# Kernel optimization log

Hardware: AMD Instinct MI355X
Metric: run time of the kernel (lower is better)

## Reference

```python
import jax, jax.numpy as jnp
import numpy as np

GAMMA = 0.05
EPS = 1e-12
H, NH, HD = 768, 12, 64

def _lin(x, W, b):
    return x @ W.T + b

def _pproc(x, W, b):
    # LRP gamma-rule projection: forward value equals _lin(x, W, b); gradient flows through the gamma-modified layer times a detached ratio.
    z = _lin(x, W, b)
    zp = _lin(x, W + GAMMA * jnp.clip(W, 0.0, None), b + GAMMA * jnp.clip(b, 0.0, None))
    return zp * jax.lax.stop_gradient(z / zp)

def setup_inputs() -> dict:
    key = jax.random.key(0)
    ks = jax.random.split(key, 9)
    s = 0.02
    d = {"hidden_states": jax.random.normal(ks[0], (2, 2048, H), jnp.float32)}
    for i, n in enumerate(["q", "k", "v", "o"]):
        d["W" + n] = jax.random.normal(ks[1 + 2 * i], (H, H), jnp.float32) * s
        d["b" + n] = jax.random.normal(ks[2 + 2 * i], (H,), jnp.float32) * s
    return d

def reference(hidden_states, Wq, bq, Wk, bk, Wv, bv, Wo, bo):
    B, S, _ = hidden_states.shape
    def heads(x):  # [B,S,H] -> [B,NH,S,HD]
        return x.reshape(B, S, NH, HD).transpose(0, 2, 1, 3)
    q = heads(_pproc(hidden_states, Wq, bq))
    k = heads(_pproc(hidden_states, Wk, bk))
    v = heads(_pproc(hidden_states, Wv, bv))
    # NOTE: source has NO 1/sqrt(d_head) scaling on the scores
    scores = jnp.einsum("bhsd,bhtd->bhst", q, k)
    probs = jax.lax.stop_gradient(jax.nn.softmax(scores, axis=-1))  # detach_kq branch
    ctx = jnp.einsum("bhst,bhtd->bhsd", probs, v).transpose(0, 2, 1, 3).reshape(B, S, H)
    # BertSelfOutput.pforward: gamma-modified dense applied directly (no pproc ratio)
    pWo = Wo + GAMMA * jnp.clip(Wo, 0.0, None)
    pbo = bo + GAMMA * jnp.clip(bo, 0.0, None)
    y = _lin(ctx, pWo, pbo) + hidden_states
    # 'nowb' LayerNorm with detached mean and std (torch.std -> unbiased, ddof=1)
    mean = jax.lax.stop_gradient(jnp.mean(y, axis=-1, keepdims=True))
    std = jax.lax.stop_gradient(jnp.std(y, axis=-1, keepdims=True, ddof=1))
    out = (y - mean) / (std + EPS)
    return out, probs
```

## Files before the change

kernel.cpp:

```cpp
#include <hip/hip_runtime.h>

#define GAMMA 0.05f
#define LNEPS 1e-12f
#define HDIMT 768
#define SDIM  2048
#define NHEAD 12
#define HDHEAD 64
#define MTOT  4096
#define BHEADS 24
#define OUT0E ((size_t)MTOT * HDIMT)
#define NXEL  ((size_t)MTOT * HDIMT)
#define WNEL  ((size_t)HDIMT * HDIMT)
#define NEATT ((size_t)BHEADS * SDIM * HDHEAD)

typedef __attribute__((ext_vector_type(8))) short short8;
typedef __attribute__((ext_vector_type(4))) float f32x4;
typedef __attribute__((ext_vector_type(16))) float f32x16;

#define MFMA16(a, b, c) __builtin_amdgcn_mfma_f32_16x16x32_bf16((a), (b), (c), 0, 0, 0)
#define MFMA32(a, b, c) __builtin_amdgcn_mfma_f32_32x32x16_bf16((a), (b), (c), 0, 0, 0)

__device__ __forceinline__ float bf2f(unsigned short u) {
    union { unsigned int i; float f; } c; c.i = ((unsigned int)u) << 16; return c.f;
}
__device__ __forceinline__ unsigned short f2bf(float f) {
    union { float f; unsigned int i; } c; c.f = f;
    unsigned int i = c.i;
    i += 0x7FFFu + ((i >> 16) & 1u);
    return (unsigned short)(i >> 16);
}
__device__ __forceinline__ void splitbf(float v, unsigned short& h, unsigned short& l) {
    h = f2bf(v);
    l = f2bf(v - bf2f(h));
}

__device__ __forceinline__ void load8f(const void* p, size_t idx, int isbf, float* r) {
    if (isbf) {
        const unsigned short* b = (const unsigned short*)p + idx;
        uint4 u = *(const uint4*)b;
        const unsigned short* pu = (const unsigned short*)&u;
        #pragma unroll
        for (int j = 0; j < 8; ++j) r[j] = bf2f(pu[j]);
    } else {
        const float* f = (const float*)p + idx;
        float4 a = *(const float4*)f, c = *(const float4*)(f + 4);
        r[0] = a.x; r[1] = a.y; r[2] = a.z; r[3] = a.w;
        r[4] = c.x; r[5] = c.y; r[6] = c.z; r[7] = c.w;
    }
}
__device__ __forceinline__ float load1f(const void* p, size_t idx, int isbf) {
    return isbf ? bf2f(((const unsigned short*)p)[idx]) : ((const float*)p)[idx];
}

__global__ void detect_kernel(const void* __restrict__ x, int* __restrict__ flag) {
    __shared__ int cnt;
    if (threadIdx.x == 0) cnt = 0;
    __syncthreads();
    const unsigned short* u = (const unsigned short*)x;
    unsigned short v = u[2 * threadIdx.x];
    int e = (v >> 7) & 0xFF;
    int ok = (e >= 100 && e <= 140) ? 1 : 0;
    atomicAdd(&cnt, ok);
    __syncthreads();
    if (threadIdx.x == 0) flag[0] = (cnt >= 192) ? 1 : 0;
}

__global__ __launch_bounds__(256) void prep_kernel(
    const void* __restrict__ x,
    const void* __restrict__ Wq, const void* __restrict__ Wk,
    const void* __restrict__ Wv, const void* __restrict__ Wo,
    unsigned short* __restrict__ xh, unsigned short* __restrict__ xl,
    unsigned short* __restrict__ wqh, unsigned short* __restrict__ wql,
    unsigned short* __restrict__ wkh, unsigned short* __restrict__ wkl,
    unsigned short* __restrict__ wvh, unsigned short* __restrict__ wvl,
    unsigned short* __restrict__ woh, unsigned short* __restrict__ wol,
    const int* __restrict__ flag)
{
    const int isbf = flag[0];
    const int z = blockIdx.y;
    const size_t i8 = ((size_t)blockIdx.x * 256 + threadIdx.x) * 8;
    const void* src; unsigned short* dh; unsigned short* dl;
    size_t n; int gam = 0;
    if (z == 0)      { src = x;  dh = xh;  dl = xl;  n = NXEL; }
    else if (z == 1) { src = Wq; dh = wqh; dl = wql; n = WNEL; }
    else if (z == 2) { src = Wk; dh = wkh; dl = wkl; n = WNEL; }
    else if (z == 3) { src = Wv; dh = wvh; dl = wvl; n = WNEL; }
    else             { src = Wo; dh = woh; dl = wol; n = WNEL; gam = 1; }
    if (i8 >= n) return;

    float v[8]; load8f(src, i8, isbf, v);
    alignas(16) unsigned short hv[8], lv[8];
    #pragma unroll
    for (int j = 0; j < 8; ++j) {
        float f = v[j];
        if (gam) f += GAMMA * fmaxf(f, 0.0f);
        splitbf(f, hv[j], lv[j]);
    }
    *(uint4*)(dh + i8) = *(const uint4*)hv;
    *(uint4*)(dl + i8) = *(const uint4*)lv;
}

#define FRAG(buf, row, kb)                                                        \
    (*(const short8*)((const char*)(buf) +                                        \
                      (((row) << 7) + ((kb) ^ (((row) & 7) << 4)))))

__global__ __launch_bounds__(256) void qkv_mfma(
    const unsigned short* __restrict__ xh, const unsigned short* __restrict__ xl,
    const unsigned short* __restrict__ wqh, const unsigned short* __restrict__ wql,
    const unsigned short* __restrict__ wkh, const unsigned short* __restrict__ wkl,
    const unsigned short* __restrict__ wvh, const unsigned short* __restrict__ wvl,
    const void* __restrict__ bq, const void* __restrict__ bk, const void* __restrict__ bv,
    unsigned short* __restrict__ qh, unsigned short* __restrict__ ql,
    unsigned short* __restrict__ kh, unsigned short* __restrict__ kl,
    unsigned short* __restrict__ vth,
    const int* __restrict__ flag)
{
    __shared__ alignas(16) unsigned short Ah[8192], Al[8192];
    __shared__ alignas(16) unsigned short Bh[4096], Bl[4096];

    const int isbf = flag[0];
    const int tid = threadIdx.x;
    const int lane = tid & 63, w = tid >> 6;
    const int l15 = lane & 15, g = lane >> 4;
    const int m0 = blockIdx.x * 128;
    const int h  = blockIdx.y;
    const int z  = blockIdx.z;

    const unsigned short* Wh = (z == 0) ? wqh : (z == 1) ? wkh : wvh;
    const unsigned short* Wl = (z == 0) ? wql : (z == 1) ? wkl : wvl;
    const void* bias = (z == 0) ? bq : (z == 1) ? bk : bv;

    f32x4 acc[2][4];
    #pragma unroll
    for (int i = 0; i < 2; ++i)
        #pragma unroll
        for (int c = 0; c < 4; ++c) acc[i][c] = (f32x4){0.0f, 0.0f, 0.0f, 0.0f};

    for (int k0 = 0; k0 < HDIMT; k0 += 64) {
        __syncthreads();
        #pragma unroll
        for (int p = 0; p < 4; ++p) {
            const int idx = tid + p * 256;
            const int row = idx >> 3, slot = idx & 7;
            const int off = (row << 7) + ((slot << 4) ^ ((row & 7) << 4));
            const size_t s = (size_t)(m0 + row) * HDIMT + k0 + slot * 8;
            *(uint4*)((char*)Ah + off) = *(const uint4*)(xh + s);
            *(uint4*)((char*)Al + off) = *(const uint4*)(xl + s);
        }
        #pragma unroll
        for (int p = 0; p < 2; ++p) {
            const int idx = tid + p * 256;
            const int row = idx >> 3, slot = idx & 7;
            const int off = (row << 7) + ((slot << 4) ^ ((row & 7) << 4));
            const size_t s = (size_t)(h * 64 + row) * HDIMT + k0 + slot * 8;
            *(uint4*)((char*)Bh + off) = *(const uint4*)(Wh + s);
            *(uint4*)((char*)Bl + off) = *(const uint4*)(Wl + s);
        }
        __syncthreads();

        #pragma unroll
        for (int ks = 0; ks < 2; ++ks) {
            const int kb = (g << 4) + (ks << 6);
            short8 a8h[2], a8l[2], b8h[4], b8l[4];
            #pragma unroll
            for (int i = 0; i < 2; ++i) {
                const int row = w * 32 + i * 16 + l15;
                a8h[i] = FRAG(Ah, row, kb);
                a8l[i] = FRAG(Al, row, kb);
            }
            #pragma unroll
            for (int c = 0; c < 4; ++c) {
                const int row = c * 16 + l15;
                b8h[c] = FRAG(Bh, row, kb);
                b8l[c] = FRAG(Bl, row, kb);
            }
            #pragma unroll
            for (int i = 0; i < 2; ++i)
                #pragma unroll
                for (int c = 0; c < 4; ++c) {
                    acc[i][c] = MFMA16(a8h[i], b8h[c], acc[i][c]);
                    acc[i][c] = MFMA16(a8l[i], b8h[c], acc[i][c]);
                    acc[i][c] = MFMA16(a8h[i], b8l[c], acc[i][c]);
                }
        }
    }

    float bb[4];
    #pragma unroll
    for (int c = 0; c < 4; ++c) bb[c] = load1f(bias, h * 64 + c * 16 + l15, isbf);

    if (z < 2) {
        unsigned short* oh = z ? kh : qh;
        unsigned short* ol = z ? kl : ql;
        #pragma unroll
        for (int i = 0; i < 2; ++i)
            #pragma unroll
            for (int c = 0; c < 4; ++c)
                #pragma unroll
                for (int r = 0; r < 4; ++r) {
                    const int m = m0 + w * 32 + i * 16 + g * 4 + r;
                    const int b = m >> 11, s = m & 2047;
                    const int d = c * 16 + l15;
                    unsigned short hu, lu;
                    splitbf(acc[i][c][r] + bb[c], hu, lu);
                    const size_t o = ((size_t)(b * NHEAD + h) * SDIM + s) * HDHEAD + d;
                    oh[o] = hu; ol[o] = lu;
                }
    } else {
        #pragma unroll
        for (int i = 0; i < 2; ++i)
            #pragma unroll
            for (int c = 0; c < 4; ++c) {
                const int m00 = m0 + w * 32 + i * 16 + g * 4;
                const int b = m00 >> 11, s0 = m00 & 2047;
                const int d = c * 16 + l15;
                ushort4 hv;
                unsigned short* hp = (unsigned short*)&hv;
                #pragma unroll
                for (int r = 0; r < 4; ++r) hp[r] = f2bf(acc[i][c][r] + bb[c]);
                const size_t o = ((size_t)(b * NHEAD + h) * HDHEAD + d) * SDIM + s0;
                *(ushort4*)(vth + o) = hv;
            }
    }
}

#define STAGE64(dsth, dstl, srch, srcl, SROW)                                     \
    {                                                                             \
        _Pragma("unroll")                                                         \
        for (int p_ = 0; p_ < 2; ++p_) {                                          \
            const int idx_ = tid + p_ * 256;                                      \
            const int row_ = idx_ >> 3, slot_ = idx_ & 7;                         \
            const int off_ = (row_ << 7) + ((slot_ << 4) ^ ((row_ & 7) << 4));    \
            *(uint4*)((char*)(dsth) + off_) =                                     \
                *(const uint4*)((srch) + (size_t)row_ * (SROW) + slot_ * 8);      \
            *(uint4*)((char*)(dstl) + off_) =                                     \
                *(const uint4*)((srcl) + (size_t)row_ * (SROW) + slot_ * 8);      \
        }                                                                         \
    }

#define STAGE64H(dst, src, SROW)                                                  \
    {                                                                             \
        _Pragma("unroll")                                                         \
        for (int p_ = 0; p_ < 2; ++p_) {                                          \
            const int idx_ = tid + p_ * 256;                                      \
            const int row_ = idx_ >> 3, slot_ = idx_ & 7;                         \
            const int off_ = (row_ << 7) + ((slot_ << 4) ^ ((row_ & 7) << 4));    \
            *(uint4*)((char*)(dst) + off_) =                                      \
                *(const uint4*)((src) + (size_t)row_ * (SROW) + slot_ * 8);       \
        }                                                                         \
    }

__global__ __launch_bounds__(256) void attn_kernel(
    const unsigned short* __restrict__ qh, const unsigned short* __restrict__ ql,
    const unsigned short* __restrict__ kh, const unsigned short* __restrict__ kl,
    const unsigned short* __restrict__ vth,
    unsigned short* __restrict__ ctxh, unsigned short* __restrict__ ctxl,
    void* __restrict__ dout,
    const int* __restrict__ flag)
{
    __shared__ alignas(16) unsigned short Qh[4096], Ql[4096];
    __shared__ alignas(16) unsigned short Kh[4096], Kl[4096];
    __shared__ alignas(16) unsigned short Vh[4096];
    __shared__ alignas(16) unsigned short Ph[4096];
    __shared__ float lsums[64][2];
    __shared__ float linv[64];

    const int isbf = flag[0];
    const int tid  = threadIdx.x;
    const int lane = tid & 63;
    const int w    = tid >> 6;
    const int l31  = lane & 31, g2 = lane >> 5;
    const int qh_  = (w >> 1) * 32;
    const int th_  = (w & 1) * 32;
    const int bh   = blockIdx.y;
    const int r0   = blockIdx.x * 64;

    const unsigned short* kbh = kh + (size_t)bh * SDIM * HDHEAD;
    const unsigned short* kbl = kl + (size_t)bh * SDIM * HDHEAD;
    const unsigned short* vb  = vth + (size_t)bh * HDHEAD * SDIM;

    {
        const unsigned short* sh = qh + ((size_t)bh * SDIM + r0) * HDHEAD;
        const unsigned short* sl = ql + ((size_t)bh * SDIM + r0) * HDHEAD;
        STAGE64(Qh, Ql, sh, sl, HDHEAD);
    }
    __syncthreads();

    short8 aqh[4], aql[4];
    #pragma unroll
    for (int ks = 0; ks < 4; ++ks) {
        const int kb = ks * 32 + g2 * 16;
        aqh[ks] = FRAG(Qh, qh_ + l31, kb);
        aql[ks] = FRAG(Ql, qh_ + l31, kb);
    }

    float lsum[16];
    #pragma unroll
    for (int r = 0; r < 16; ++r) lsum[r] = 0.0f;

    STAGE64H(Kh, kbh, HDHEAD);
    for (int kt = 0; kt < 32; ++kt) {
        __syncthreads();
        unsigned short* cur = (kt & 1) ? Kl : Kh;
        unsigned short* nxt = (kt & 1) ? Kh : Kl;
        if (kt < 31) STAGE64H(nxt, kbh + (size_t)(kt + 1) * 64 * HDHEAD, HDHEAD);

        f32x16 acc = {};
        #pragma unroll
        for (int ks = 0; ks < 4; ++ks) {
            const int kb = ks * 32 + g2 * 16;
            short8 b8 = FRAG(cur, th_ + l31, kb);
            acc = MFMA32(aqh[ks], b8, acc);
            acc = MFMA32(aql[ks], b8, acc);
        }
        #pragma unroll
        for (int r = 0; r < 16; ++r) lsum[r] += __expf(acc[r]);
    }

    #pragma unroll
    for (int d = 1; d < 32; d <<= 1) {
        #pragma unroll
        for (int r = 0; r < 16; ++r) lsum[r] += __shfl_xor(lsum[r], d, 64);
    }
    if (l31 == 0) {
        #pragma unroll
        for (int r = 0; r < 16; ++r) {
            const int qrow = qh_ + (r & 3) + 8 * (r >> 2) + 4 * g2;
            lsums[qrow][w & 1] = lsum[r];
        }
    }
    __syncthreads();
    if (tid < 64) linv[tid] = 1.0f / (lsums[tid][0] + lsums[tid][1]);
    __syncthreads();

    float invr[16];
    #pragma unroll
    for (int r = 0; r < 16; ++r)
        invr[r] = linv[qh_ + (r & 3) + 8 * (r >> 2) + 4 * g2];

    f32x16 cacc = {};
    const size_t grow = OUT0E + ((size_t)bh * SDIM + r0) * SDIM;

    for (int kt = 0; kt < 32; ++kt) {
        __syncthreads();
        STAGE64(Kh, Kl, kbh + (size_t)kt * 64 * HDHEAD,
                        kbl + (size_t)kt * 64 * HDHEAD, HDHEAD);
        STAGE64H(Vh, vb + (size_t)(kt * 64), SDIM);
        __syncthreads();

        f32x16 acc = {};
        #pragma unroll
        for (int ks = 0; ks < 4; ++ks) {
            const int kb = ks * 32 + g2 * 16;
            short8 b8h = FRAG(Kh, th_ + l31, kb);
            short8 b8l = FRAG(Kl, th_ + l31, kb);
            acc = MFMA32(aqh[ks], b8h, acc);
            acc = MFMA32(aql[ks], b8h, acc);
            acc = MFMA32(aqh[ks], b8l, acc);
        }

        const int tcol = th_ + l31;
        const int gcol = kt * 64 + tcol;
        #pragma unroll
        for (int r = 0; r < 16; ++r) {
            const float p = __expf(acc[r]) * invr[r];
            const int q = qh_ + (r & 3) + 8 * (r >> 2) + 4 * g2;
            if (isbf) ((unsigned short*)dout)[grow + (size_t)q * SDIM + gcol] = f2bf(p);
            else      ((float*)dout)[grow + (size_t)q * SDIM + gcol] = p;
            const int off = (q << 7) + ((tcol << 1) ^ ((q & 7) << 4));
            *(unsigned short*)((char*)Ph + off) = f2bf(p);
        }
        __syncthreads();

        #pragma unroll
        for (int ks = 0; ks < 4; ++ks) {
            const int kb = ks * 32 + g2 * 16;
            short8 pa = FRAG(Ph, qh_ + l31, kb);
            short8 v8 = FRAG(Vh, th_ + l31, kb);
            cacc = MFMA32(pa, v8, cacc);
        }
    }

    const int bb_ = bh / NHEAD, hh_ = bh % NHEAD;
    #pragma unroll
    for (int r = 0; r < 16; ++r) {
        const int q = qh_ + (r & 3) + 8 * (r >> 2) + 4 * g2;
        const int d = th_ + l31;
        unsigned short hu, lu;
        splitbf(cacc[r], hu, lu);
        const size_t o = ((size_t)(bb_ * SDIM + r0 + q)) * HDIMT + hh_ * HDHEAD + d;
        ctxh[o] = hu; ctxl[o] = lu;
    }
}

__global__ __launch_bounds__(256) void oproj_mfma(
    const unsigned short* __restrict__ ctxh, const unsigned short* __restrict__ ctxl,
    const unsigned short* __restrict__ woh, const unsigned short* __restrict__ wol,
    const void* __restrict__ bo, const void* __restrict__ x,
    float* __restrict__ y, const int* __restrict__ flag)
{
    __shared__ alignas(16) unsigned short Ah[8192], Al[8192];
    __shared__ alignas(16) unsigned short Bh[4096], Bl[4096];

    const int isbf = flag[0];
    const int tid = threadIdx.x;
    const int lane = tid & 63, w = tid >> 6;
    const int l15 = lane & 15, g = lane >> 4;
    const int m0 = blockIdx.x * 128;
    const int h  = blockIdx.y;

    f32x4 acc[2][4];
    #pragma unroll
    for (int i = 0; i < 2; ++i)
        #pragma unroll
        for (int c = 0; c < 4; ++c) acc[i][c] = (f32x4){0.0f, 0.0f, 0.0f, 0.0f};

    for (int k0 = 0; k0 < HDIMT; k0 += 64) {
        __syncthreads();
        #pragma unroll
        for (int p = 0; p < 4; ++p) {
            const int idx = tid + p * 256;
            const int row = idx >> 3, slot = idx & 7;
            const int off = (row << 7) + ((slot << 4) ^ ((row & 7) << 4));
            const size_t s = (size_t)(m0 + row) * HDIMT + k0 + slot * 8;
            *(uint4*)((char*)Ah + off) = *(const uint4*)(ctxh + s);
            *(uint4*)((char*)Al + off) = *(const uint4*)(ctxl + s);
        }
        #pragma unroll
        for (int p = 0; p < 2; ++p) {
            const int idx = tid + p * 256;
            const int row = idx >> 3, slot = idx & 7;
            const int off = (row << 7) + ((slot << 4) ^ ((row & 7) << 4));
            const size_t s = (size_t)(h * 64 + row) * HDIMT + k0 + slot * 8;
            *(uint4*)((char*)Bh + off) = *(const uint4*)(woh + s);
            *(uint4*)((char*)Bl + off) = *(const uint4*)(wol + s);
        }
        __syncthreads();

        #pragma unroll
        for (int ks = 0; ks < 2; ++ks) {
            const int kb = (g << 4) + (ks << 6);
            short8 a8h[2], a8l[2], b8h[4], b8l[4];
            #pragma unroll
            for (int i = 0; i < 2; ++i) {
                const int row = w * 32 + i * 16 + l15;
                a8h[i] = FRAG(Ah, row, kb);
                a8l[i] = FRAG(Al, row, kb);
            }
            #pragma unroll
            for (int c = 0; c < 4; ++c) {
                const int row = c * 16 + l15;
                b8h[c] = FRAG(Bh, row, kb);
                b8l[c] = FRAG(Bl, row, kb);
            }
            #pragma unroll
            for (int i = 0; i < 2; ++i)
                #pragma unroll
                for (int c = 0; c < 4; ++c) {
                    acc[i][c] = MFMA16(a8h[i], b8h[c], acc[i][c]);
                    acc[i][c] = MFMA16(a8l[i], b8h[c], acc[i][c]);
                    acc[i][c] = MFMA16(a8h[i], b8l[c], acc[i][c]);
                }
        }
    }

    float pb[4];
    #pragma unroll
    for (int c = 0; c < 4; ++c) {
        float t = load1f(bo, h * 64 + c * 16 + l15, isbf);
        pb[c] = t + GAMMA * fmaxf(t, 0.0f);
    }

    #pragma unroll
    for (int i = 0; i < 2; ++i)
        #pragma unroll
        for (int c = 0; c < 4; ++c)
            #pragma unroll
            for (int r = 0; r < 4; ++r) {
                const int m = m0 + w * 32 + i * 16 + g * 4 + r;
                const int n = h * 64 + c * 16 + l15;
                const size_t o = (size_t)m * HDIMT + n;
                y[o] = acc[i][c][r] + pb[c] + load1f(x, o, isbf);
            }
}

__global__ __launch_bounds__(256) void ln_kernel(
    const float* __restrict__ y, void* __restrict__ out,
    const int* __restrict__ flag)
{
    __shared__ float part[8];
    const int isbf = flag[0];
    const int m = blockIdx.x;
    const int tid = threadIdx.x;
    const int lane = tid & 63, w = tid >> 6;
    const float* yr = y + (size_t)m * HDIMT;

    float v0 = yr[tid], v1 = yr[tid + 256], v2 = yr[tid + 512];

    float s = v0 + v1 + v2;
    #pragma unroll
    for (int d = 1; d < 64; d <<= 1) s += __shfl_xor(s, d, 64);
    if (lane == 0) part[w] = s;
    __syncthreads();
    const float mean = (part[0] + part[1] + part[2] + part[3]) * (1.0f / 768.0f);

    const float d0 = v0 - mean, d1 = v1 - mean, d2 = v2 - mean;
    float ss = d0 * d0 + d1 * d1 + d2 * d2;
    #pragma unroll
    for (int d = 1; d < 64; d <<= 1) ss += __shfl_xor(ss, d, 64);
    if (lane == 0) part[4 + w] = ss;
    __syncthreads();
    const float var = (part[4] + part[5] + part[6] + part[7]) * (1.0f / 767.0f);
    const float inv = 1.0f / (sqrtf(var) + LNEPS);

    const size_t base = (size_t)m * HDIMT;
    if (isbf) {
        unsigned short* o = (unsigned short*)out;
        o[base + tid]       = f2bf(d0 * inv);
        o[base + tid + 256] = f2bf(d1 * inv);
        o[base + tid + 512] = f2bf(d2 * inv);
    } else {
        float* o = (float*)out;
        o[base + tid]       = d0 * inv;
        o[base + tid + 256] = d1 * inv;
        o[base + tid + 512] = d2 * inv;
    }
}

extern "C" void kernel_launch(void* const* d_in, const int* in_sizes, int n_in,
                              void* d_out, int out_size, void* d_ws, size_t ws_size,
                              hipStream_t stream)
{
    (void)in_sizes; (void)n_in; (void)out_size; (void)ws_size;

    const void* x  = d_in[0];
    const void* Wq = d_in[1];
    const void* bq = d_in[2];
    const void* Wk = d_in[3];
    const void* bk = d_in[4];
    const void* Wv = d_in[5];
    const void* bv = d_in[6];
    const void* Wo = d_in[7];
    const void* bo = d_in[8];

    unsigned short* qh  = (unsigned short*)d_ws;
    unsigned short* ql  = qh  + NEATT;
    unsigned short* kh  = ql  + NEATT;
    unsigned short* kl  = kh  + NEATT;
    unsigned short* vth = kl  + NEATT;
    unsigned short* xh  = vth + NEATT;
    unsigned short* xl  = xh  + NXEL;
    unsigned short* wqh = xl  + NXEL;
    unsigned short* wql = wqh + WNEL;
    unsigned short* wkh = wql + WNEL;
    unsigned short* wkl = wkh + WNEL;
    unsigned short* wvh = wkl + WNEL;
    unsigned short* wvl = wvh + WNEL;
    unsigned short* woh = wvl + WNEL;
    unsigned short* wol = woh + WNEL;
    int* flag = (int*)(wol + WNEL);

    float* y = (float*)qh;
    unsigned short* ctxh = xh;
    unsigned short* ctxl = xl;

    detect_kernel<<<1, 256, 0, stream>>>(x, flag);
    prep_kernel<<<dim3(1536, 5), 256, 0, stream>>>(x, Wq, Wk, Wv, Wo,
                                                   xh, xl, wqh, wql, wkh, wkl,
                                                   wvh, wvl, woh, wol, flag);
    qkv_mfma<<<dim3(32, 12, 3), 256, 0, stream>>>(xh, xl, wqh, wql, wkh, wkl, wvh, wvl,
                                                  bq, bk, bv,
                                                  qh, ql, kh, kl, vth, flag);
    attn_kernel<<<dim3(32, 24), 256, 0, stream>>>(qh, ql, kh, kl, vth,
                                                  ctxh, ctxl, d_out, flag);
    oproj_mfma<<<dim3(32, 12), 256, 0, stream>>>(ctxh, ctxl, woh, wol, bo, x, y, flag);
    ln_kernel<<<MTOT, 256, 0, stream>>>(y, d_out, flag);
}
```

Baseline: 772.2 us.

## Register-prefetch K/V tiles, load Q directly, fold normalization into exp

In the attention kernel's second pass, the next K-high, K-low and V tiles are now loaded from global memory into registers while the current tile is computed, then written to shared memory after the PV MFMAs. Previously the kernel staged each tile synchronously between two barriers. Q fragments are read straight from global memory into registers, which drops the Q shared buffers and a barrier and lowers LDS use. The launch bounds now request 4 blocks per CU. The softmax normalization is folded into the exponent as a negative log-sum, and the hi/lo MFMA chains are split into two accumulators for more ILP. The costs are extra registers for the prefetched data and slightly different rounding in the probabilities.

```diff
diff --git a/kernel.cpp b/kernel.cpp
--- a/kernel.cpp
+++ b/kernel.cpp
@@ -224,97 +224,81 @@
     }
 }
 
-#define STAGE64(dsth, dstl, srch, srcl, SROW)                                     \
-    {                                                                             \
-        _Pragma("unroll")                                                         \
-        for (int p_ = 0; p_ < 2; ++p_) {                                          \
-            const int idx_ = tid + p_ * 256;                                      \
-            const int row_ = idx_ >> 3, slot_ = idx_ & 7;                         \
-            const int off_ = (row_ << 7) + ((slot_ << 4) ^ ((row_ & 7) << 4));    \
-            *(uint4*)((char*)(dsth) + off_) =                                     \
-                *(const uint4*)((srch) + (size_t)row_ * (SROW) + slot_ * 8);      \
-            *(uint4*)((char*)(dstl) + off_) =                                     \
-                *(const uint4*)((srcl) + (size_t)row_ * (SROW) + slot_ * 8);      \
-        }                                                                         \
-    }
-
-#define STAGE64H(dst, src, SROW)                                                  \
-    {                                                                             \
-        _Pragma("unroll")                                                         \
-        for (int p_ = 0; p_ < 2; ++p_) {                                          \
-            const int idx_ = tid + p_ * 256;                                      \
-            const int row_ = idx_ >> 3, slot_ = idx_ & 7;                         \
-            const int off_ = (row_ << 7) + ((slot_ << 4) ^ ((row_ & 7) << 4));    \
-            *(uint4*)((char*)(dst) + off_) =                                      \
-                *(const uint4*)((src) + (size_t)row_ * (SROW) + slot_ * 8);       \
-        }                                                                         \
-    }
-
-__global__ __launch_bounds__(256) void attn_kernel(
-    const unsigned short* __restrict__ qh, const unsigned short* __restrict__ ql,
-    const unsigned short* __restrict__ kh, const unsigned short* __restrict__ kl,
-    const unsigned short* __restrict__ vth,
+__global__ __launch_bounds__(256, 4) void attn_kernel(
+    const unsigned short* __restrict__ qhp, const unsigned short* __restrict__ qlp,
+    const unsigned short* __restrict__ khp, const unsigned short* __restrict__ klp,
+    const unsigned short* __restrict__ vtp,
     unsigned short* __restrict__ ctxh, unsigned short* __restrict__ ctxl,
     void* __restrict__ dout,
     const int* __restrict__ flag)
 {
-    __shared__ alignas(16) unsigned short Qh[4096], Ql[4096];
     __shared__ alignas(16) unsigned short Kh[4096], Kl[4096];
     __shared__ alignas(16) unsigned short Vh[4096];
     __shared__ alignas(16) unsigned short Ph[4096];
     __shared__ float lsums[64][2];
-    __shared__ float linv[64];
+    __shared__ float lml[64];
 
     const int isbf = flag[0];
     const int tid  = threadIdx.x;
     const int lane = tid & 63;
     const int w    = tid >> 6;
     const int l31  = lane & 31, g2 = lane >> 5;
-    const int qh_  = (w >> 1) * 32;
+    const int qt_  = (w >> 1) * 32;
     const int th_  = (w & 1) * 32;
     const int bh   = blockIdx.y;
     const int r0   = blockIdx.x * 64;
 
-    const unsigned short* kbh = kh + (size_t)bh * SDIM * HDHEAD;
-    const unsigned short* kbl = kl + (size_t)bh * SDIM * HDHEAD;
-    const unsigned short* vb  = vth + (size_t)bh * HDHEAD * SDIM;
+    const unsigned short* kbh = khp + (size_t)bh * SDIM * HDHEAD;
+    const unsigned short* kbl = klp + (size_t)bh * SDIM * HDHEAD;
+    const unsigned short* vb  = vtp + (size_t)bh * HDHEAD * SDIM;
+
+    const int sr0 = tid >> 3, ss0 = tid & 7;
+    const int sr1 = sr0 + 32;
+    const int soff0 = (sr0 << 7) + ((ss0 << 4) ^ ((sr0 & 7) << 4));
+    const int soff1 = (sr1 << 7) + ((ss0 << 4) ^ ((sr1 & 7) << 4));
+    const size_t kof0 = (size_t)sr0 * HDHEAD + ss0 * 8;
+    const size_t kof1 = (size_t)sr1 * HDHEAD + ss0 * 8;
+    const size_t vof0 = (size_t)sr0 * SDIM + ss0 * 8;
+    const size_t vof1 = (size_t)sr1 * SDIM + ss0 * 8;
+
+    const unsigned short* qrh = qhp + ((size_t)bh * SDIM + r0 + qt_ + l31) * HDHEAD + g2 * 8;
+    const unsigned short* qrl = qlp + ((size_t)bh * SDIM + r0 + qt_ + l31) * HDHEAD + g2 * 8;
+    short8 aqh[4], aql[4];
+    #pragma unroll
+    for (int ks = 0; ks < 4; ++ks) {
+        aqh[ks] = *(const short8*)(qrh + ks * 16);
+        aql[ks] = *(const short8*)(qrl + ks * 16);
+    }
+
+    float lsum[16];
+    #pragma unroll
+    for (int r = 0; r < 16; ++r) lsum[r] = 0.0f;
 
     {
-        const unsigned short* sh = qh + ((size_t)bh * SDIM + r0) * HDHEAD;
-        const unsigned short* sl = ql + ((size_t)bh * SDIM + r0) * HDHEAD;
-        STAGE64(Qh, Ql, sh, sl, HDHEAD);
-    }
-    __syncthreads();
-
-    short8 aqh[4], aql[4];
-    #pragma unroll
-    for (int ks = 0; ks < 4; ++ks) {
-        const int kb = ks * 32 + g2 * 16;
-        aqh[ks] = FRAG(Qh, qh_ + l31, kb);
-        aql[ks] = FRAG(Ql, qh_ + l31, kb);
-    }
-
-    float lsum[16];
-    #pragma unroll
-    for (int r = 0; r < 16; ++r) lsum[r] = 0.0f;
-
-    STAGE64H(Kh, kbh, HDHEAD);
+        uint4 a = *(const uint4*)(kbh + kof0), b = *(const uint4*)(kbh + kof1);
+        *(uint4*)((char*)Kh + soff0) = a;
+        *(uint4*)((char*)Kh + soff1) = b;
+    }
     for (int kt = 0; kt < 32; ++kt) {
         __syncthreads();
-        unsigned short* cur = (kt & 1) ? Kl : Kh;
+        const unsigned short* cur = (kt & 1) ? Kl : Kh;
         unsigned short* nxt = (kt & 1) ? Kh : Kl;
-        if (kt < 31) STAGE64H(nxt, kbh + (size_t)(kt + 1) * 64 * HDHEAD, HDHEAD);
-
-        f32x16 acc = {};
+        if (kt < 31) {
+            const unsigned short* src = kbh + (size_t)(kt + 1) * 64 * HDHEAD;
+            uint4 a = *(const uint4*)(src + kof0), b = *(const uint4*)(src + kof1);
+            *(uint4*)((char*)nxt + soff0) = a;
+            *(uint4*)((char*)nxt + soff1) = b;
+        }
+        f32x16 c1 = {}, c2 = {};
         #pragma unroll
         for (int ks = 0; ks < 4; ++ks) {
             const int kb = ks * 32 + g2 * 16;
             short8 b8 = FRAG(cur, th_ + l31, kb);
-            acc = MFMA32(aqh[ks], b8, acc);
-            acc = MFMA32(aql[ks], b8, acc);
-        }
-        #pragma unroll
-        for (int r = 0; r < 16; ++r) lsum[r] += __expf(acc[r]);
+            c1 = MFMA32(aqh[ks], b8, c1);
+            c2 = MFMA32(aql[ks], b8, c2);
+        }
+        #pragma unroll
+        for (int r = 0; r < 16; ++r) lsum[r] += __expf(c1[r] + c2[r]);
     }
 
     #pragma unroll
@@ -325,46 +309,52 @@
     if (l31 == 0) {
         #pragma unroll
         for (int r = 0; r < 16; ++r) {
-            const int qrow = qh_ + (r & 3) + 8 * (r >> 2) + 4 * g2;
+            const int qrow = qt_ + (r & 3) + 8 * (r >> 2) + 4 * g2;
             lsums[qrow][w & 1] = lsum[r];
         }
     }
     __syncthreads();
-    if (tid < 64) linv[tid] = 1.0f / (lsums[tid][0] + lsums[tid][1]);
-    __syncthreads();
-
-    float invr[16];
-    #pragma unroll
-    for (int r = 0; r < 16; ++r)
-        invr[r] = linv[qh_ + (r & 3) + 8 * (r >> 2) + 4 * g2];
+    if (tid < 64) lml[tid] = -__logf(lsums[tid][0] + lsums[tid][1]);
+    __syncthreads();
 
     f32x16 cacc = {};
     const size_t grow = OUT0E + ((size_t)bh * SDIM + r0) * SDIM;
 
+    uint4 pkh0 = *(const uint4*)(kbh + kof0), pkh1 = *(const uint4*)(kbh + kof1);
+    uint4 pkl0 = *(const uint4*)(kbl + kof0), pkl1 = *(const uint4*)(kbl + kof1);
+    uint4 pv0  = *(const uint4*)(vb + vof0),  pv1  = *(const uint4*)(vb + vof1);
+    *(uint4*)((char*)Kh + soff0) = pkh0;  *(uint4*)((char*)Kh + soff1) = pkh1;
+    *(uint4*)((char*)Kl + soff0) = pkl0;  *(uint4*)((char*)Kl + soff1) = pkl1;
+    *(uint4*)((char*)Vh + soff0) = pv0;   *(uint4*)((char*)Vh + soff1) = pv1;
+    __syncthreads();
+
     for (int kt = 0; kt < 32; ++kt) {
-        __syncthreads();
-        STAGE64(Kh, Kl, kbh + (size_t)kt * 64 * HDHEAD,
-                        kbl + (size_t)kt * 64 * HDHEAD, HDHEAD);
-        STAGE64H(Vh, vb + (size_t)(kt * 64), SDIM);
-        __syncthreads();
-
-        f32x16 acc = {};
+        if (kt < 31) {
+            const unsigned short* ksrc = kbh + (size_t)(kt + 1) * 64 * HDHEAD;
+            const unsigned short* lsrc = kbl + (size_t)(kt + 1) * 64 * HDHEAD;
+            const unsigned short* vsrc = vb + (size_t)((kt + 1) * 64);
+            pkh0 = *(const uint4*)(ksrc + kof0);  pkh1 = *(const uint4*)(ksrc + kof1);
+            pkl0 = *(const uint4*)(lsrc + kof0);  pkl1 = *(const uint4*)(lsrc + kof1);
+            pv0  = *(const uint4*)(vsrc + vof0);  pv1  = *(const uint4*)(vsrc + vof1);
+        }
+
+        f32x16 c1 = {}, c2 = {};
         #pragma unroll
         for (int ks = 0; ks < 4; ++ks) {
             const int kb = ks * 32 + g2 * 16;
             short8 b8h = FRAG(Kh, th_ + l31, kb);
             short8 b8l = FRAG(Kl, th_ + l31, kb);
-            acc = MFMA32(aqh[ks], b8h, acc);
-            acc = MFMA32(aql[ks], b8h, acc);
-            acc = MFMA32(aqh[ks], b8l, acc);
+            c1 = MFMA32(aqh[ks], b8h, c1);
+            c2 = MFMA32(aql[ks], b8h, c2);
+            c2 = MFMA32(aqh[ks], b8l, c2);
         }
 
         const int tcol = th_ + l31;
         const int gcol = kt * 64 + tcol;
         #pragma unroll
         for (int r = 0; r < 16; ++r) {
-            const float p = __expf(acc[r]) * invr[r];
-            const int q = qh_ + (r & 3) + 8 * (r >> 2) + 4 * g2;
+            const int q = qt_ + (r & 3) + 8 * (r >> 2) + 4 * g2;
+            const float p = __expf(c1[r] + c2[r] + lml[q]);
             if (isbf) ((unsigned short*)dout)[grow + (size_t)q * SDIM + gcol] = f2bf(p);
             else      ((float*)dout)[grow + (size_t)q * SDIM + gcol] = p;
             const int off = (q << 7) + ((tcol << 1) ^ ((q & 7) << 4));
@@ -375,16 +365,24 @@
         #pragma unroll
         for (int ks = 0; ks < 4; ++ks) {
             const int kb = ks * 32 + g2 * 16;
-            short8 pa = FRAG(Ph, qh_ + l31, kb);
+            short8 pa = FRAG(Ph, qt_ + l31, kb);
             short8 v8 = FRAG(Vh, th_ + l31, kb);
             cacc = MFMA32(pa, v8, cacc);
         }
+        __syncthreads();
+
+        if (kt < 31) {
+            *(uint4*)((char*)Kh + soff0) = pkh0;  *(uint4*)((char*)Kh + soff1) = pkh1;
+            *(uint4*)((char*)Kl + soff0) = pkl0;  *(uint4*)((char*)Kl + soff1) = pkl1;
+            *(uint4*)((char*)Vh + soff0) = pv0;   *(uint4*)((char*)Vh + soff1) = pv1;
+            __syncthreads();
+        }
     }
 
     const int bb_ = bh / NHEAD, hh_ = bh % NHEAD;
     #pragma unroll
     for (int r = 0; r < 16; ++r) {
-        const int q = qh_ + (r & 3) + 8 * (r >> 2) + 4 * g2;
+        const int q = qt_ + (r & 3) + 8 * (r >> 2) + 4 * g2;
         const int d = th_ + l31;
         unsigned short hu, lu;
         splitbf(cacc[r], hu, lu);
```

After: 919.6 us. 19.1% more time.
